# Optimization experiments

Measured on AMD Instinct MI355X. Metric: run time of the kernel, lower is better.

The kernel has to match this reference:

```python
import jax, jax.numpy as jnp
import numpy as np
from math import sqrt

D_MODEL = 1024
N_HEADS = 16
E = D_MODEL // N_HEADS  # d_keys = d_values = 64


def setup_inputs() -> dict:
    key = jax.random.key(0)
    ks = jax.random.split(key, 11)
    B, L, S = 2, 2048, 2048
    s = 1.0 / sqrt(D_MODEL)
    return {
        "queries": jax.random.normal(ks[0], (B, L, D_MODEL), jnp.float32),
        "keys": jax.random.normal(ks[1], (B, S, D_MODEL), jnp.float32),
        "values": jax.random.normal(ks[2], (B, S, D_MODEL), jnp.float32),
        "Wq": jax.random.normal(ks[3], (D_MODEL, D_MODEL), jnp.float32) * s,
        "bq": jnp.zeros((D_MODEL,), jnp.float32),
        "Wk": jax.random.normal(ks[4], (D_MODEL, D_MODEL), jnp.float32) * s,
        "bk": jnp.zeros((D_MODEL,), jnp.float32),
        "Wv": jax.random.normal(ks[5], (D_MODEL, D_MODEL), jnp.float32) * s,
        "bv": jnp.zeros((D_MODEL,), jnp.float32),
        "Wo": jax.random.normal(ks[6], (D_MODEL, D_MODEL), jnp.float32) * s,
        "bo": jnp.zeros((D_MODEL,), jnp.float32),
    }


def reference(queries, keys, values, Wq, bq, Wk, bk, Wv, bv, Wo, bo):
    B, L, _ = queries.shape
    S = keys.shape[1]
    H = N_HEADS
    # projections -> [B, L/S, H, E]
    q = (queries @ Wq + bq).reshape(B, L, H, E)
    k = (keys @ Wk + bk).reshape(B, S, H, E)
    v = (values @ Wv + bv).reshape(B, S, H, E)
    scale = 1.0 / sqrt(E)
    scores = jnp.einsum('blhe,bshe->bhls', q, k)  # [B,H,L,S]
    A = jax.nn.softmax(scale * scores, axis=-1)   # dropout = identity (eval)
    V = jnp.einsum('bhls,bshd->blhd', A, v)       # [B,L,H,E]
    out = V.reshape(B, L, H * E) @ Wo + bo
    return out
```

## Files before the change

kernel.cpp:

```cpp
#include <hip/hip_runtime.h>
#include <hip/hip_bf16.h>
#include <stdint.h>

#define BATCH 2
#define SEQ   2048
#define DM    1024
#define NH    16
#define EH    64
#define MROWS (BATCH*SEQ)

typedef __attribute__((ext_vector_type(8))) short  short8;
typedef __attribute__((ext_vector_type(4))) float  floatx4;
typedef __attribute__((ext_vector_type(8))) unsigned short ushort8v;
typedef __attribute__((ext_vector_type(4))) unsigned short ushort4v;

__device__ __forceinline__ unsigned short f2bf(float f) {
    return (unsigned short)((__float_as_uint(f) + 0x8000u) >> 16);
}

__device__ __forceinline__ void gload_lds16(const void* g, void* l) {
    __builtin_amdgcn_global_load_lds(
        (const __attribute__((address_space(1))) unsigned int*)g,
        (__attribute__((address_space(3))) unsigned int*)l, 16, 0, 0);
}

__global__ __launch_bounds__(256)
void transpose_w(const float* __restrict__ W0, const float* __restrict__ W1,
                 const float* __restrict__ W2, const float* __restrict__ W3,
                 unsigned short* __restrict__ T0, unsigned short* __restrict__ T1,
                 unsigned short* __restrict__ T2, unsigned short* __restrict__ T3,
                 int zbase)
{
    int z = zbase + blockIdx.z;
    const float* W = (z == 0) ? W0 : (z == 1) ? W1 : (z == 2) ? W2 : W3;
    unsigned short* T = (z == 0) ? T0 : (z == 1) ? T1 : (z == 2) ? T2 : T3;
    __shared__ float t[32][33];
    const int tid = threadIdx.x;
    const int k0 = blockIdx.y * 32, n0 = blockIdx.x * 32;
    {
        int r = tid >> 3, c4 = (tid & 7) * 4;
        float4 u = *(const float4*)&W[(size_t)(k0 + r) * DM + n0 + c4];
        t[r][c4 + 0] = u.x; t[r][c4 + 1] = u.y; t[r][c4 + 2] = u.z; t[r][c4 + 3] = u.w;
    }
    __syncthreads();
    {
        int n = tid >> 3, k4 = (tid & 7) * 4;
        ushort4v o;
        o[0] = f2bf(t[k4 + 0][n]); o[1] = f2bf(t[k4 + 1][n]);
        o[2] = f2bf(t[k4 + 2][n]); o[3] = f2bf(t[k4 + 3][n]);
        *(ushort4v*)&T[(size_t)(n0 + n) * DM + k0 + k4] = o;
    }
}

struct ProjArgs {
    const float* act[3];
    const unsigned short* wt[3];
    const float* bias[3];
    unsigned short* C[3];
    float oscale[3];
};

__global__ __launch_bounds__(256)
void proj_qkv(ProjArgs pa)
{
    const int z = blockIdx.z;
    const bool vt = (z == 2);
    const int linear = (int)(blockIdx.x + gridDim.x * blockIdx.y);
    int rb, cb;
    if (!vt) { rb = linear & 31; cb = linear >> 5; }
    else     { cb = linear & 31; rb = linear >> 5; }
    const int row0 = rb * 128, col0 = cb * 128;

    const float* act = pa.act[z];
    const unsigned short* wt = pa.wt[z];

    __shared__ unsigned short As[128 * 32];
    __shared__ unsigned short Bs[128 * 32];

    const int tid = threadIdx.x;
    const int lane = tid & 63, w = tid >> 6;
    const int lane15 = lane & 15, quad = lane >> 4;

    floatx4 acc[2][8] = {};

    for (int kt = 0; kt < DM; kt += 32) {
        __syncthreads();
        if (!vt) {
#pragma unroll
            for (int rr = 0; rr < 2; ++rr) {
                int c = rr * 256 + tid;
                int row = c >> 2, kel = (c & 3) * 8;
                const float* p = &act[(size_t)(row0 + row) * DM + kt + kel];
                float4 u0 = *(const float4*)p;
                float4 u1 = *(const float4*)(p + 4);
                ushort8v o8;
                o8[0] = f2bf(u0.x); o8[1] = f2bf(u0.y); o8[2] = f2bf(u0.z); o8[3] = f2bf(u0.w);
                o8[4] = f2bf(u1.x); o8[5] = f2bf(u1.y); o8[6] = f2bf(u1.z); o8[7] = f2bf(u1.w);
                *(ushort8v*)&As[(size_t)c * 8] = o8;
            }
#pragma unroll
            for (int rr = 0; rr < 2; ++rr) {
                int c = rr * 256 + w * 64 + lane;
                int row = c >> 2, kel = (c & 3) * 8;
                gload_lds16(&wt[(size_t)(col0 + row) * DM + kt + kel],
                            (char*)Bs + (size_t)(rr * 256 + w * 64) * 16);
            }
        } else {
#pragma unroll
            for (int rr = 0; rr < 2; ++rr) {
                int c = rr * 256 + w * 64 + lane;
                int row = c >> 2, kel = (c & 3) * 8;
                gload_lds16(&wt[(size_t)(row0 + row) * DM + kt + kel],
                            (char*)As + (size_t)(rr * 256 + w * 64) * 16);
            }
#pragma unroll
            for (int rr = 0; rr < 2; ++rr) {
                int c = rr * 256 + tid;
                int row = c >> 2, kel = (c & 3) * 8;
                const float* p = &act[(size_t)(col0 + row) * DM + kt + kel];
                float4 u0 = *(const float4*)p;
                float4 u1 = *(const float4*)(p + 4);
                ushort8v o8;
                o8[0] = f2bf(u0.x); o8[1] = f2bf(u0.y); o8[2] = f2bf(u0.z); o8[3] = f2bf(u0.w);
                o8[4] = f2bf(u1.x); o8[5] = f2bf(u1.y); o8[6] = f2bf(u1.z); o8[7] = f2bf(u1.w);
                *(ushort8v*)&Bs[(size_t)c * 8] = o8;
            }
        }
        __syncthreads();

        short8 af[2], bf[8];
#pragma unroll
        for (int i = 0; i < 2; ++i)
            af[i] = *(const short8*)&As[(w * 32 + i * 16 + lane15) * 32 + quad * 8];
#pragma unroll
        for (int j = 0; j < 8; ++j)
            bf[j] = *(const short8*)&Bs[(j * 16 + lane15) * 32 + quad * 8];
#pragma unroll
        for (int i = 0; i < 2; ++i)
#pragma unroll
            for (int j = 0; j < 8; ++j)
                acc[i][j] = __builtin_amdgcn_mfma_f32_16x16x32_bf16(af[i], bf[j], acc[i][j], 0, 0, 0);
    }

    const float* bias = pa.bias[z];
    const float os = pa.oscale[z];
    unsigned short* C = pa.C[z];
#pragma unroll
    for (int i = 0; i < 2; ++i) {
#pragma unroll
        for (int j = 0; j < 8; ++j) {
#pragma unroll
            for (int r = 0; r < 4; ++r) {
                int row = row0 + w * 32 + i * 16 + quad * 4 + r;
                int col = col0 + j * 16 + lane15;
                if (!vt) {
                    float v = (acc[i][j][r] + bias[col]) * os;
                    int b = row >> 11, l = row & (SEQ - 1);
                    int h = col >> 6,  e = col & (EH - 1);
                    C[((size_t)(b * NH + h) * SEQ + l) * EH + e] = f2bf(v);
                } else {
                    float v = acc[i][j][r] + bias[row];
                    int h = row >> 6,  e = row & (EH - 1);
                    int b = col >> 11, l = col & (SEQ - 1);
                    C[((size_t)(b * NH + h) * EH + e) * SEQ + l] = f2bf(v);
                }
            }
        }
    }
}

__global__ __launch_bounds__(256)
void gemm_out(const unsigned short* __restrict__ ctx,
              const unsigned short* __restrict__ WoT,
              const float* __restrict__ bo,
              float* __restrict__ out)
{
    const int linear = (int)(blockIdx.x + gridDim.x * blockIdx.y);
    const int rb = linear & 31, cb = linear >> 5;
    const int row0 = rb * 128, col0 = cb * 64;

    __shared__ unsigned short As[128 * 32];
    __shared__ unsigned short Bs[64 * 32];

    const int tid = threadIdx.x;
    const int lane = tid & 63, w = tid >> 6;
    const int lane15 = lane & 15, quad = lane >> 4;

    floatx4 acc[2][4] = {};

    for (int kt = 0; kt < DM; kt += 32) {
        __syncthreads();
#pragma unroll
        for (int rr = 0; rr < 2; ++rr) {
            int c = rr * 256 + w * 64 + lane;
            int row = c >> 2, kel = (c & 3) * 8;
            gload_lds16(&ctx[(size_t)(row0 + row) * DM + kt + kel],
                        (char*)As + (size_t)(rr * 256 + w * 64) * 16);
        }
        {
            int c = w * 64 + lane;
            int row = c >> 2, kel = (c & 3) * 8;
            gload_lds16(&WoT[(size_t)(col0 + row) * DM + kt + kel],
                        (char*)Bs + (size_t)(w * 64) * 16);
        }
        __syncthreads();

        short8 af[2], bf[4];
#pragma unroll
        for (int i = 0; i < 2; ++i)
            af[i] = *(const short8*)&As[(w * 32 + i * 16 + lane15) * 32 + quad * 8];
#pragma unroll
        for (int j = 0; j < 4; ++j)
            bf[j] = *(const short8*)&Bs[(j * 16 + lane15) * 32 + quad * 8];
#pragma unroll
        for (int i = 0; i < 2; ++i)
#pragma unroll
            for (int j = 0; j < 4; ++j)
                acc[i][j] = __builtin_amdgcn_mfma_f32_16x16x32_bf16(af[i], bf[j], acc[i][j], 0, 0, 0);
    }

#pragma unroll
    for (int i = 0; i < 2; ++i)
#pragma unroll
        for (int j = 0; j < 4; ++j)
#pragma unroll
            for (int r = 0; r < 4; ++r) {
                int row = row0 + w * 32 + i * 16 + quad * 4 + r;
                int col = col0 + j * 16 + lane15;
                out[(size_t)row * DM + col] = acc[i][j][r] + bo[col];
            }
}

__device__ __forceinline__ void stage_kv(const unsigned short* __restrict__ Kp,
                                         const unsigned short* __restrict__ Vp,
                                         int st, unsigned short* ksb, unsigned short* vsb,
                                         int w, int lane)
{
#pragma unroll
    for (int rr = 0; rr < 2; ++rr) {
        int p = rr * 256 + w * 64 + lane;
        int row = p >> 3;
        int gch = (p & 7) ^ (row & 7);
        gload_lds16(&Kp[(size_t)(st + row) * EH + gch * 8],
                    ksb + (size_t)(rr * 256 + w * 64) * 8);
        gload_lds16(&Vp[(size_t)row * SEQ + st + gch * 8],
                    vsb + (size_t)(rr * 256 + w * 64) * 8);
    }
}

__global__ __launch_bounds__(256)
void attn_mfma(const unsigned short* __restrict__ Qh,
               const unsigned short* __restrict__ Kh,
               const unsigned short* __restrict__ Vt,
               unsigned short* __restrict__ ctx)
{
    __shared__ unsigned short Ks[2][64 * 64];
    __shared__ unsigned short Vs[2][64 * 64];
    __shared__ unsigned short Ps[128][72];

    const int tid = threadIdx.x;
    const int lane = tid & 63, w = tid >> 6;
    const int lane15 = lane & 15, quad = lane >> 4;
    const int qt = blockIdx.x, h = blockIdx.y, b = blockIdx.z;
    const size_t bh = (size_t)(b * NH + h);
    const unsigned short* Kp = Kh + bh * SEQ * EH;
    const unsigned short* Vp = Vt + bh * EH * SEQ;

    short8 qf[2][2];
    {
        const unsigned short* Qp =
            Qh + (bh * SEQ + (size_t)qt * 128 + w * 32 + lane15) * EH;
#pragma unroll
        for (int ks = 0; ks < 2; ++ks) {
            qf[0][ks] = *(const short8*)(Qp + ks * 32 + quad * 8);
            qf[1][ks] = *(const short8*)(Qp + 16 * EH + ks * 32 + quad * 8);
        }
    }
    short8 ones;
#pragma unroll
    for (int i = 0; i < 8; ++i) ones[i] = (short)0x3F80;

    floatx4 o[2][4] = {};
    floatx4 lacc[2] = {};

    stage_kv(Kp, Vp, 0, Ks[0], Vs[0], w, lane);
    __syncthreads();
    int cur = 0;

    for (int st = 0; st < SEQ; st += 64) {
        int nxt = cur ^ 1;
        if (st + 64 < SEQ)
            stage_kv(Kp, Vp, st + 64, Ks[nxt], Vs[nxt], w, lane);
        const unsigned short* ksb = Ks[cur];
        const unsigned short* vsb = Vs[cur];

        floatx4 sacc[4][2] = {};
#pragma unroll
        for (int ts = 0; ts < 4; ++ts) {
#pragma unroll
            for (int ks = 0; ks < 2; ++ks) {
                short8 kf = *(const short8*)&ksb[((ts * 16 + lane15) << 6) +
                                                 ((((ks << 2) + quad) ^ (lane15 & 7)) << 3)];
                sacc[ts][0] = __builtin_amdgcn_mfma_f32_16x16x32_bf16(kf, qf[0][ks], sacc[ts][0], 0, 0, 0);
                sacc[ts][1] = __builtin_amdgcn_mfma_f32_16x16x32_bf16(kf, qf[1][ks], sacc[ts][1], 0, 0, 0);
            }
        }

#pragma unroll
        for (int ts = 0; ts < 4; ++ts)
#pragma unroll
            for (int nq = 0; nq < 2; ++nq) {
                unsigned int u0 = __float_as_uint(__builtin_amdgcn_exp2f(sacc[ts][nq][0])) + 0x8000u;
                unsigned int u1 = __float_as_uint(__builtin_amdgcn_exp2f(sacc[ts][nq][1])) + 0x8000u;
                unsigned int u2 = __float_as_uint(__builtin_amdgcn_exp2f(sacc[ts][nq][2])) + 0x8000u;
                unsigned int u3 = __float_as_uint(__builtin_amdgcn_exp2f(sacc[ts][nq][3])) + 0x8000u;
                uint2 pk;
                pk.x = (u0 >> 16) | (u1 & 0xFFFF0000u);
                pk.y = (u2 >> 16) | (u3 & 0xFFFF0000u);
                *(uint2*)&Ps[w * 32 + nq * 16 + lane15][ts * 16 + quad * 4] = pk;
            }

#pragma unroll
        for (int ks = 0; ks < 2; ++ks) {
            short8 pf[2];
#pragma unroll
            for (int mt = 0; mt < 2; ++mt) {
                pf[mt] = *(const short8*)&Ps[w * 32 + mt * 16 + lane15][ks * 32 + quad * 8];
                lacc[mt] = __builtin_amdgcn_mfma_f32_16x16x32_bf16(pf[mt], ones, lacc[mt], 0, 0, 0);
            }
#pragma unroll
            for (int t2 = 0; t2 < 4; ++t2) {
                short8 vf = *(const short8*)&vsb[((t2 * 16 + lane15) << 6) +
                                                 ((((ks << 2) + quad) ^ (lane15 & 7)) << 3)];
                o[0][t2] = __builtin_amdgcn_mfma_f32_16x16x32_bf16(pf[0], vf, o[0][t2], 0, 0, 0);
                o[1][t2] = __builtin_amdgcn_mfma_f32_16x16x32_bf16(pf[1], vf, o[1][t2], 0, 0, 0);
            }
        }
        __syncthreads();
        cur = nxt;
    }

#pragma unroll
    for (int mt = 0; mt < 2; ++mt) {
        float inv[4];
#pragma unroll
        for (int r = 0; r < 4; ++r) inv[r] = 1.0f / lacc[mt][r];
#pragma unroll
        for (int t2 = 0; t2 < 4; ++t2)
#pragma unroll
            for (int r = 0; r < 4; ++r) {
                int q = qt * 128 + w * 32 + mt * 16 + quad * 4 + r;
                int col = h * EH + t2 * 16 + lane15;
                ctx[((size_t)(b * SEQ + q)) * DM + col] = f2bf(o[mt][t2][r] * inv[r]);
            }
    }
}

extern "C" void kernel_launch(void* const* d_in, const int* in_sizes, int n_in,
                              void* d_out, int out_size, void* d_ws, size_t ws_size,
                              hipStream_t stream)
{
    const float* queries = (const float*)d_in[0];
    const float* keys    = (const float*)d_in[1];
    const float* values  = (const float*)d_in[2];
    const float* Wq = (const float*)d_in[3];
    const float* bq = (const float*)d_in[4];
    const float* Wk = (const float*)d_in[5];
    const float* bk = (const float*)d_in[6];
    const float* Wv = (const float*)d_in[7];
    const float* bv = (const float*)d_in[8];
    const float* Wo = (const float*)d_in[9];
    const float* bo = (const float*)d_in[10];
    float* out = (float*)d_out;

    unsigned short* ws = (unsigned short*)d_ws;
    const size_t MAT = (size_t)MROWS * DM;
    const size_t WSZ = (size_t)DM * DM;
    unsigned short* Qhp = ws;
    unsigned short* Khp = ws + MAT;
    unsigned short* Vtp = ws + 2 * MAT;
    unsigned short* ctx = ws + 3 * MAT;
    unsigned short* WqT = ctx;
    unsigned short* WkT = ctx + WSZ;
    unsigned short* WvT = ctx + 2 * WSZ;
    unsigned short* WoT = ws;

    const float qscale = 0.125f * 1.44269504088896f;

    transpose_w<<<dim3(DM / 32, DM / 32, 3), 256, 0, stream>>>(
        Wq, Wk, Wv, Wo, WqT, WkT, WvT, WoT, 0);

    ProjArgs pa;
    pa.act[0] = queries; pa.act[1] = keys; pa.act[2] = values;
    pa.wt[0] = WqT;      pa.wt[1] = WkT;   pa.wt[2] = WvT;
    pa.bias[0] = bq;     pa.bias[1] = bk;  pa.bias[2] = bv;
    pa.C[0] = Qhp;       pa.C[1] = Khp;    pa.C[2] = Vtp;
    pa.oscale[0] = qscale; pa.oscale[1] = 1.f; pa.oscale[2] = 1.f;
    proj_qkv<<<dim3(8, 32, 3), 256, 0, stream>>>(pa);

    attn_mfma<<<dim3(SEQ / 128, NH, BATCH), 256, 0, stream>>>(Qhp, Khp, Vtp, ctx);

    transpose_w<<<dim3(DM / 32, DM / 32, 1), 256, 0, stream>>>(
        Wq, Wk, Wv, Wo, WqT, WkT, WvT, WoT, 3);

    gemm_out<<<dim3(16, 32), 256, 0, stream>>>(ctx, WoT, bo, out);
}
```

Before: 245.5 us.

## Pre-convert K/V to bf16, widen GEMM k-tile to 64 with XOR swizzle

Adds a separate kernel that converts keys and values to bf16 up front, so the K and V projections can stream both operands with direct global-to-LDS loads instead of converting fp32 inside the GEMM. Both GEMMs now use a 64-wide k-tile with an XOR-swizzled LDS layout to halve barrier count and avoid bank conflicts. All four weight transposes are merged into one launch, and the workspace is reorganized so Q/K are parked in the output buffer. The attention grid is also remapped so consecutive blocks cover different heads. This costs an extra pass over K/V in memory and doubles LDS per block, which may reduce occupancy.

```diff
diff --git a/kernel.cpp b/kernel.cpp
--- a/kernel.cpp
+++ b/kernel.cpp
@@ -25,13 +25,27 @@
 }
 
 __global__ __launch_bounds__(256)
+void convert_kv(const float* __restrict__ K, const float* __restrict__ V,
+                unsigned short* __restrict__ Kbf, unsigned short* __restrict__ Vbf)
+{
+    const float* src = blockIdx.z ? V : K;
+    unsigned short* dst = blockIdx.z ? Vbf : Kbf;
+    size_t i = ((size_t)blockIdx.x * 256 + threadIdx.x) * 8;
+    float4 u0 = *(const float4*)&src[i];
+    float4 u1 = *(const float4*)&src[i + 4];
+    ushort8v o8;
+    o8[0] = f2bf(u0.x); o8[1] = f2bf(u0.y); o8[2] = f2bf(u0.z); o8[3] = f2bf(u0.w);
+    o8[4] = f2bf(u1.x); o8[5] = f2bf(u1.y); o8[6] = f2bf(u1.z); o8[7] = f2bf(u1.w);
+    *(ushort8v*)&dst[i] = o8;
+}
+
+__global__ __launch_bounds__(256)
 void transpose_w(const float* __restrict__ W0, const float* __restrict__ W1,
                  const float* __restrict__ W2, const float* __restrict__ W3,
                  unsigned short* __restrict__ T0, unsigned short* __restrict__ T1,
-                 unsigned short* __restrict__ T2, unsigned short* __restrict__ T3,
-                 int zbase)
-{
-    int z = zbase + blockIdx.z;
+                 unsigned short* __restrict__ T2, unsigned short* __restrict__ T3)
+{
+    int z = blockIdx.z;
     const float* W = (z == 0) ? W0 : (z == 1) ? W1 : (z == 2) ? W2 : W3;
     unsigned short* T = (z == 0) ? T0 : (z == 1) ? T1 : (z == 2) ? T2 : T3;
     __shared__ float t[32][33];
@@ -53,11 +67,13 @@
 }
 
 struct ProjArgs {
-    const float* act[3];
+    const float* queries;
+    const unsigned short* Kbf;
+    const unsigned short* Vbf;
     const unsigned short* wt[3];
     const float* bias[3];
     unsigned short* C[3];
-    float oscale[3];
+    float qscale;
 };
 
 __global__ __launch_bounds__(256)
@@ -71,11 +87,11 @@
     else     { cb = linear & 31; rb = linear >> 5; }
     const int row0 = rb * 128, col0 = cb * 128;
 
-    const float* act = pa.act[z];
-    const unsigned short* wt = pa.wt[z];
-
-    __shared__ unsigned short As[128 * 32];
-    __shared__ unsigned short Bs[128 * 32];
+    const unsigned short* aSrc = (z == 1) ? pa.Kbf : pa.wt[2];
+    const unsigned short* bSrc = (z == 0) ? pa.wt[0] : (z == 1) ? pa.wt[1] : pa.Vbf;
+
+    __shared__ unsigned short As[128 * 64];
+    __shared__ unsigned short Bs[128 * 64];
 
     const int tid = threadIdx.x;
     const int lane = tid & 63, w = tid >> 6;
@@ -83,67 +99,62 @@
 
     floatx4 acc[2][8] = {};
 
-    for (int kt = 0; kt < DM; kt += 32) {
+    for (int kt = 0; kt < DM; kt += 64) {
         __syncthreads();
-        if (!vt) {
-#pragma unroll
-            for (int rr = 0; rr < 2; ++rr) {
-                int c = rr * 256 + tid;
-                int row = c >> 2, kel = (c & 3) * 8;
-                const float* p = &act[(size_t)(row0 + row) * DM + kt + kel];
-                float4 u0 = *(const float4*)p;
-                float4 u1 = *(const float4*)(p + 4);
+        if (z == 0) {
+#pragma unroll
+            for (int rr = 0; rr < 4; ++rr) {
+                int p = rr * 256 + tid;
+                int row = p >> 3, gch = (p & 7) ^ (row & 7);
+                const float* s = &pa.queries[(size_t)(row0 + row) * DM + kt + gch * 8];
+                float4 u0 = *(const float4*)s;
+                float4 u1 = *(const float4*)(s + 4);
                 ushort8v o8;
                 o8[0] = f2bf(u0.x); o8[1] = f2bf(u0.y); o8[2] = f2bf(u0.z); o8[3] = f2bf(u0.w);
                 o8[4] = f2bf(u1.x); o8[5] = f2bf(u1.y); o8[6] = f2bf(u1.z); o8[7] = f2bf(u1.w);
-                *(ushort8v*)&As[(size_t)c * 8] = o8;
-            }
-#pragma unroll
-            for (int rr = 0; rr < 2; ++rr) {
-                int c = rr * 256 + w * 64 + lane;
-                int row = c >> 2, kel = (c & 3) * 8;
-                gload_lds16(&wt[(size_t)(col0 + row) * DM + kt + kel],
-                            (char*)Bs + (size_t)(rr * 256 + w * 64) * 16);
+                *(ushort8v*)&As[(size_t)p * 8] = o8;
             }
         } else {
 #pragma unroll
-            for (int rr = 0; rr < 2; ++rr) {
-                int c = rr * 256 + w * 64 + lane;
-                int row = c >> 2, kel = (c & 3) * 8;
-                gload_lds16(&wt[(size_t)(row0 + row) * DM + kt + kel],
+            for (int rr = 0; rr < 4; ++rr) {
+                int p = rr * 256 + w * 64 + lane;
+                int row = p >> 3, gch = (p & 7) ^ (row & 7);
+                gload_lds16(&aSrc[(size_t)(row0 + row) * DM + kt + gch * 8],
                             (char*)As + (size_t)(rr * 256 + w * 64) * 16);
             }
-#pragma unroll
-            for (int rr = 0; rr < 2; ++rr) {
-                int c = rr * 256 + tid;
-                int row = c >> 2, kel = (c & 3) * 8;
-                const float* p = &act[(size_t)(col0 + row) * DM + kt + kel];
-                float4 u0 = *(const float4*)p;
-                float4 u1 = *(const float4*)(p + 4);
-                ushort8v o8;
-                o8[0] = f2bf(u0.x); o8[1] = f2bf(u0.y); o8[2] = f2bf(u0.z); o8[3] = f2bf(u0.w);
-                o8[4] = f2bf(u1.x); o8[5] = f2bf(u1.y); o8[6] = f2bf(u1.z); o8[7] = f2bf(u1.w);
-                *(ushort8v*)&Bs[(size_t)c * 8] = o8;
-            }
+        }
+#pragma unroll
+        for (int rr = 0; rr < 4; ++rr) {
+            int p = rr * 256 + w * 64 + lane;
+            int row = p >> 3, gch = (p & 7) ^ (row & 7);
+            gload_lds16(&bSrc[(size_t)(col0 + row) * DM + kt + gch * 8],
+                        (char*)Bs + (size_t)(rr * 256 + w * 64) * 16);
         }
         __syncthreads();
 
-        short8 af[2], bf[8];
-#pragma unroll
-        for (int i = 0; i < 2; ++i)
-            af[i] = *(const short8*)&As[(w * 32 + i * 16 + lane15) * 32 + quad * 8];
-#pragma unroll
-        for (int j = 0; j < 8; ++j)
-            bf[j] = *(const short8*)&Bs[(j * 16 + lane15) * 32 + quad * 8];
-#pragma unroll
-        for (int i = 0; i < 2; ++i)
-#pragma unroll
-            for (int j = 0; j < 8; ++j)
-                acc[i][j] = __builtin_amdgcn_mfma_f32_16x16x32_bf16(af[i], bf[j], acc[i][j], 0, 0, 0);
+#pragma unroll
+        for (int ks = 0; ks < 2; ++ks) {
+            short8 af[2], bf[8];
+#pragma unroll
+            for (int i = 0; i < 2; ++i) {
+                int r = w * 32 + i * 16 + lane15;
+                af[i] = *(const short8*)&As[r * 64 + (((ks * 4 + quad) ^ (r & 7)) << 3)];
+            }
+#pragma unroll
+            for (int j = 0; j < 8; ++j) {
+                int r = j * 16 + lane15;
+                bf[j] = *(const short8*)&Bs[r * 64 + (((ks * 4 + quad) ^ (r & 7)) << 3)];
+            }
+#pragma unroll
+            for (int i = 0; i < 2; ++i)
+#pragma unroll
+                for (int j = 0; j < 8; ++j)
+                    acc[i][j] = __builtin_amdgcn_mfma_f32_16x16x32_bf16(af[i], bf[j], acc[i][j], 0, 0, 0);
+        }
     }
 
     const float* bias = pa.bias[z];
-    const float os = pa.oscale[z];
+    const float os = (z == 0) ? pa.qscale : 1.f;
     unsigned short* C = pa.C[z];
 #pragma unroll
     for (int i = 0; i < 2; ++i) {
@@ -179,8 +190,8 @@
     const int rb = linear & 31, cb = linear >> 5;
     const int row0 = rb * 128, col0 = cb * 64;
 
-    __shared__ unsigned short As[128 * 32];
-    __shared__ unsigned short Bs[64 * 32];
+    __shared__ unsigned short As[128 * 64];
+    __shared__ unsigned short Bs[64 * 64];
 
     const int tid = threadIdx.x;
     const int lane = tid & 63, w = tid >> 6;
@@ -188,35 +199,43 @@
 
     floatx4 acc[2][4] = {};
 
-    for (int kt = 0; kt < DM; kt += 32) {
+    for (int kt = 0; kt < DM; kt += 64) {
         __syncthreads();
 #pragma unroll
+        for (int rr = 0; rr < 4; ++rr) {
+            int p = rr * 256 + w * 64 + lane;
+            int row = p >> 3, gch = (p & 7) ^ (row & 7);
+            gload_lds16(&ctx[(size_t)(row0 + row) * DM + kt + gch * 8],
+                        (char*)As + (size_t)(rr * 256 + w * 64) * 16);
+        }
+#pragma unroll
         for (int rr = 0; rr < 2; ++rr) {
-            int c = rr * 256 + w * 64 + lane;
-            int row = c >> 2, kel = (c & 3) * 8;
-            gload_lds16(&ctx[(size_t)(row0 + row) * DM + kt + kel],
-                        (char*)As + (size_t)(rr * 256 + w * 64) * 16);
-        }
-        {
-            int c = w * 64 + lane;
-            int row = c >> 2, kel = (c & 3) * 8;
-            gload_lds16(&WoT[(size_t)(col0 + row) * DM + kt + kel],
-                        (char*)Bs + (size_t)(w * 64) * 16);
+            int p = rr * 256 + w * 64 + lane;
+            int row = p >> 3, gch = (p & 7) ^ (row & 7);
+            gload_lds16(&WoT[(size_t)(col0 + row) * DM + kt + gch * 8],
+                        (char*)Bs + (size_t)(rr * 256 + w * 64) * 16);
         }
         __syncthreads();
 
-        short8 af[2], bf[4];
-#pragma unroll
-        for (int i = 0; i < 2; ++i)
-            af[i] = *(const short8*)&As[(w * 32 + i * 16 + lane15) * 32 + quad * 8];
-#pragma unroll
-        for (int j = 0; j < 4; ++j)
-            bf[j] = *(const short8*)&Bs[(j * 16 + lane15) * 32 + quad * 8];
-#pragma unroll
-        for (int i = 0; i < 2; ++i)
-#pragma unroll
-            for (int j = 0; j < 4; ++j)
-                acc[i][j] = __builtin_amdgcn_mfma_f32_16x16x32_bf16(af[i], bf[j], acc[i][j], 0, 0, 0);
+#pragma unroll
+        for (int ks = 0; ks < 2; ++ks) {
+            short8 af[2], bf[4];
+#pragma unroll
+            for (int i = 0; i < 2; ++i) {
+                int r = w * 32 + i * 16 + lane15;
+                af[i] = *(const short8*)&As[r * 64 + (((ks * 4 + quad) ^ (r & 7)) << 3)];
+            }
+#pragma unroll
+            for (int j = 0; j < 4; ++j) {
+                int r = j * 16 + lane15;
+                bf[j] = *(const short8*)&Bs[r * 64 + (((ks * 4 + quad) ^ (r & 7)) << 3)];
+            }
+#pragma unroll
+            for (int i = 0; i < 2; ++i)
+#pragma unroll
+                for (int j = 0; j < 4; ++j)
+                    acc[i][j] = __builtin_amdgcn_mfma_f32_16x16x32_bf16(af[i], bf[j], acc[i][j], 0, 0, 0);
+        }
     }
 
 #pragma unroll
@@ -261,7 +280,12 @@
     const int tid = threadIdx.x;
     const int lane = tid & 63, w = tid >> 6;
     const int lane15 = lane & 15, quad = lane >> 4;
-    const int qt = blockIdx.x, h = blockIdx.y, b = blockIdx.z;
+
+    const int linear = (int)(blockIdx.x + 16 * (blockIdx.y + 16 * blockIdx.z));
+    const int bhid = linear & 31;
+    const int qt = linear >> 5;
+    const int h = bhid & 15, b = bhid >> 4;
+
     const size_t bh = (size_t)(b * NH + h);
     const unsigned short* Kp = Kh + bh * SEQ * EH;
     const unsigned short* Vp = Vt + bh * EH * SEQ;
@@ -376,32 +400,33 @@
     unsigned short* ws = (unsigned short*)d_ws;
     const size_t MAT = (size_t)MROWS * DM;
     const size_t WSZ = (size_t)DM * DM;
-    unsigned short* Qhp = ws;
-    unsigned short* Khp = ws + MAT;
+    unsigned short* Kbf = ws;
+    unsigned short* Vbf = ws + MAT;
     unsigned short* Vtp = ws + 2 * MAT;
-    unsigned short* ctx = ws + 3 * MAT;
-    unsigned short* WqT = ctx;
-    unsigned short* WkT = ctx + WSZ;
-    unsigned short* WvT = ctx + 2 * WSZ;
-    unsigned short* WoT = ws;
+    unsigned short* WqT = ws + 3 * MAT;
+    unsigned short* WkT = WqT + WSZ;
+    unsigned short* WvT = WqT + 2 * WSZ;
+    unsigned short* WoT = WqT + 3 * WSZ;
+    unsigned short* ctx = ws;
+    unsigned short* Qhp = (unsigned short*)d_out;
+    unsigned short* Khp = (unsigned short*)d_out + MAT;
 
     const float qscale = 0.125f * 1.44269504088896f;
 
-    transpose_w<<<dim3(DM / 32, DM / 32, 3), 256, 0, stream>>>(
-        Wq, Wk, Wv, Wo, WqT, WkT, WvT, WoT, 0);
+    transpose_w<<<dim3(DM / 32, DM / 32, 4), 256, 0, stream>>>(
+        Wq, Wk, Wv, Wo, WqT, WkT, WvT, WoT);
+
+    convert_kv<<<dim3(MAT / 2048, 1, 2), 256, 0, stream>>>(keys, values, Kbf, Vbf);
 
     ProjArgs pa;
-    pa.act[0] = queries; pa.act[1] = keys; pa.act[2] = values;
-    pa.wt[0] = WqT;      pa.wt[1] = WkT;   pa.wt[2] = WvT;
-    pa.bias[0] = bq;     pa.bias[1] = bk;  pa.bias[2] = bv;
-    pa.C[0] = Qhp;       pa.C[1] = Khp;    pa.C[2] = Vtp;
-    pa.oscale[0] = qscale; pa.oscale[1] = 1.f; pa.oscale[2] = 1.f;
+    pa.queries = queries; pa.Kbf = Kbf; pa.Vbf = Vbf;
+    pa.wt[0] = WqT; pa.wt[1] = WkT; pa.wt[2] = WvT;
+    pa.bias[0] = bq; pa.bias[1] = bk; pa.bias[2] = bv;
+    pa.C[0] = Qhp; pa.C[1] = Khp; pa.C[2] = Vtp;
+    pa.qscale = qscale;
     proj_qkv<<<dim3(8, 32, 3), 256, 0, stream>>>(pa);
 
     attn_mfma<<<dim3(SEQ / 128, NH, BATCH), 256, 0, stream>>>(Qhp, Khp, Vtp, ctx);
 
-    transpose_w<<<dim3(DM / 32, DM / 32, 1), 256, 0, stream>>>(
-        Wq, Wk, Wv, Wo, WqT, WkT, WvT, WoT, 3);
-
     gemm_out<<<dim3(16, 32), 256, 0, stream>>>(ctx, WoT, bo, out);
 }
```

Result: no change. 247.0 us (+0.6%).
